# Kernel tuning notes

Hardware: AMD Instinct MI355X
Metric: run time of the kernel (lower is better)

## Reference

```python
import jax, jax.numpy as jnp
import numpy as np

L = 2048      # sequence length (self.len)
DIM = 1024    # model dim
DPOS = 128    # positional encoding dim
B = 4
EPS = 1e-5


def make_pe(length, d):
    # standard sinusoidal positional encoding, shape [length, d]
    pos = np.arange(length)[:, None].astype(np.float32)
    div = np.exp(-np.arange(0, d, 2).astype(np.float32) * (np.log(10000.0) / d))
    pe = np.zeros((length, d), dtype=np.float32)
    pe[:, 0::2] = np.sin(pos * div)
    pe[:, 1::2] = np.cos(pos * div)
    return jnp.asarray(pe)


def setup_inputs() -> dict:
    key = jax.random.key(0)
    ks = jax.random.split(key, 16)
    s = lambda fan_in: 1.0 / np.sqrt(fan_in)
    inp = {
        "z": jax.random.normal(ks[0], (B, L, DIM), jnp.float32),
        "x": jax.random.normal(ks[1], (B, L, DIM), jnp.float32),
        "a": jax.random.normal(ks[2], (1,), jnp.float32),
        "pe": make_pe(L, DPOS),
        # torch Linear weights stored [out, in]
        "w_pos1": jax.random.normal(ks[3], (DPOS + DIM, DPOS), jnp.float32) * s(DPOS),
        "b_pos1": jnp.zeros((DPOS + DIM,), jnp.float32),
        "w_pos2": jax.random.normal(ks[4], (DIM, DPOS + DIM), jnp.float32) * s(DPOS + DIM),
        "b_pos2": jnp.zeros((DIM,), jnp.float32),
        "w1": jax.random.normal(ks[5], (DIM * 2, DIM), jnp.float32) * s(DIM),
        "b1": jnp.zeros((DIM * 2,), jnp.float32),
        "w2": jax.random.normal(ks[6], (DIM, DIM * 2), jnp.float32) * s(DIM * 2),
        "b2": jnp.zeros((DIM,), jnp.float32),
        "w3": jax.random.normal(ks[7], (DIM * 2, DIM), jnp.float32) * s(DIM),
        "b3": jnp.zeros((DIM * 2,), jnp.float32),
        "w4": jax.random.normal(ks[8], (DIM, DIM * 2), jnp.float32) * s(DIM * 2),
        "b4": jnp.zeros((DIM,), jnp.float32),
        "ln_g": jnp.ones((DIM,), jnp.float32),
        "ln_b": jnp.zeros((DIM,), jnp.float32),
    }
    return inp


def _layer_norm(v, g, b):
    mu = jnp.mean(v, axis=-1, keepdims=True)
    var = jnp.var(v, axis=-1, keepdims=True)
    return (v - mu) * jax.lax.rsqrt(var + EPS) * g + b


def _lin(v, w, b):
    return v @ w.T + b


def reference(z, x, a, pe, w_pos1, b_pos1, w_pos2, b_pos2,
              w1, b1, w2, b2, w3, b3, w4, b4, ln_g, ln_b):
    zn = _layer_norm(z, ln_g, ln_b)                       # [B, L, D]
    fz = jnp.fft.rfft(zn, n=2 * L, axis=1)                # [B, L+1, D] complex
    expa = jnp.exp(a)                                     # [1]
    window = jnp.exp(-jnp.arange(L, dtype=jnp.float32) * expa)  # [L]
    h = _lin(pe, w_pos1, b_pos1)                          # [L, DPOS+D]
    h = jax.nn.gelu(h, approximate=False)
    h = _lin(h, w_pos2, b_pos2)                           # [L, D] (dropout eval = id)
    wfh = jnp.fft.rfft(window[:, None] * h, n=2 * L, axis=0)  # [L+1, D]
    cwhz = jnp.fft.irfft(wfh * fz, axis=1)[:, :L, :]      # [B, L, D]
    x1 = _lin(x, w1, b1)
    x1 = jax.nn.gelu(x1, approximate=False)
    x1 = _lin(x1, w2, b2)
    x1 = x1 * cwhz + z
    y = _layer_norm(x1, ln_g, ln_b)
    y = _lin(y, w3, b3)
    y = jax.nn.gelu(y, approximate=False)
    y = _lin(y, w4, b4)
    return y + x1
```

## Files before the change

### kernel.cpp

```cpp
#include <hip/hip_runtime.h>
#include <hip/hip_bf16.h>
#include <cmath>

typedef __hip_bfloat16 bf16;
typedef __attribute__((ext_vector_type(8))) short bf16x8;
typedef __attribute__((ext_vector_type(4))) float f32x4;

static __device__ __forceinline__ float b2f(bf16 v) { return __bfloat162float(v); }
static __device__ __forceinline__ bf16 f2b(float v) { return __float2bfloat16(v); }
static __device__ __forceinline__ float us2f(unsigned short u) {
  return __uint_as_float(((unsigned)u) << 16);
}

static __device__ __forceinline__ void gl2lds16(const bf16* g, bf16* l) {
  __builtin_amdgcn_global_load_lds(
      (const __attribute__((address_space(1))) void*)g,
      (__attribute__((address_space(3))) void*)l, 16, 0, 0);
}

static __device__ __forceinline__ float gelu_fast(float v) {
  float u = v * (0.7978845608f + 0.0356774081f * v * v);
  float e = __expf(2.f * u);
  return v * (e * __frcp_rn(e + 1.f));
}

static __device__ __forceinline__ int xcd_swz(int lid, int nwg) {
  const int q = nwg >> 3, r = nwg & 7;
  const int xcd = lid & 7, loc = lid >> 3;
  const int base = (xcd < r) ? xcd * (q + 1) : r * (q + 1) + (xcd - r) * q;
  return base + loc;
}

struct CvtSegs { const float* src[7]; int blk_off[8]; };
__global__ __launch_bounds__(256) void cvt7_k(CvtSegs s, bf16* __restrict__ dst0)
{
  int b = blockIdx.x;
  int seg = 0;
#pragma unroll
  for (int i = 0; i < 6; ++i) seg += (b >= s.blk_off[i + 1]) ? 1 : 0;
  const float* src = s.src[seg] + (size_t)(b - s.blk_off[seg]) * 1024;
  bf16* dst = dst0 + (size_t)b * 1024;
  int idx = threadIdx.x * 4;
  float4 v = *(const float4*)(src + idx);
  union { bf16 bb[4]; ushort4 u; } o;
  o.bb[0] = f2b(v.x); o.bb[1] = f2b(v.y); o.bb[2] = f2b(v.z); o.bb[3] = f2b(v.w);
  *(ushort4*)(dst + idx) = o.u;
}

__global__ __launch_bounds__(256) void cvt_k(const float* __restrict__ in,
                                             bf16* __restrict__ out, int n)
{
  int idx = (blockIdx.x * 256 + threadIdx.x) * 4;
  if (idx >= n) return;
  float4 v = *(const float4*)(in + idx);
  union { bf16 b[4]; ushort4 u; } o;
  o.b[0] = f2b(v.x); o.b[1] = f2b(v.y); o.b[2] = f2b(v.z); o.b[3] = f2b(v.w);
  *(ushort4*)(out + idx) = o.u;
}

__global__ __launch_bounds__(256) void ln_k(const float* __restrict__ X, bf16* __restrict__ Y,
                                            const float* __restrict__ gamma,
                                            const float* __restrict__ beta)
{
  __shared__ float red[16];
  const int row = blockIdx.x, tid = threadIdx.x;
  float4 v = *(const float4*)(X + (size_t)row * 1024 + tid * 4);
  float s  = v.x + v.y + v.z + v.w;
  float s2 = v.x * v.x + v.y * v.y + v.z * v.z + v.w * v.w;
#pragma unroll
  for (int m = 32; m; m >>= 1) { s += __shfl_xor(s, m, 64); s2 += __shfl_xor(s2, m, 64); }
  const int wid = tid >> 6;
  if ((tid & 63) == 0) { red[wid] = s; red[wid + 8] = s2; }
  __syncthreads();
  s  = red[0] + red[1] + red[2] + red[3];
  s2 = red[8] + red[9] + red[10] + red[11];
  const float mu  = s * (1.f / 1024.f);
  const float var = s2 * (1.f / 1024.f) - mu * mu;
  const float rs  = rsqrtf(var + 1e-5f);
  float4 g = *(const float4*)(gamma + tid * 4);
  float4 bt = *(const float4*)(beta + tid * 4);
  union { bf16 b[4]; ushort4 u; } o;
  o.b[0] = f2b((v.x - mu) * rs * g.x + bt.x);
  o.b[1] = f2b((v.y - mu) * rs * g.y + bt.y);
  o.b[2] = f2b((v.z - mu) * rs * g.z + bt.z);
  o.b[3] = f2b((v.w - mu) * rs * g.w + bt.w);
  *(ushort4*)(Y + (size_t)row * 1024 + tid * 4) = o.u;
}

template<int EPI>
__global__ __launch_bounds__(256, 3) void gemm_k(
    const bf16* __restrict__ A, const bf16* __restrict__ W,
    const float* __restrict__ bias, void* __restrict__ Out,
    const void* __restrict__ aux0, const void* __restrict__ aux1,
    int M, int N, int K)
{
  __shared__ bf16 As[3][128 * 32];
  __shared__ bf16 Bs[3][128 * 32];
  const int tid = threadIdx.x;
  const int wid = tid >> 6, lane = tid & 63;
  const int quad = lane >> 4, l16 = lane & 15;
  const int wm = wid >> 1, wn = wid & 1;

  const int nwg = gridDim.x * gridDim.y;
  int lid = xcd_swz(blockIdx.y * gridDim.x + blockIdx.x, nwg);
  const int bx = lid % gridDim.x, by = lid / gridDim.x;
  const int m0 = by * 128, n0 = bx * 128;

  f32x4 acc[4][4];
#pragma unroll
  for (int i = 0; i < 4; ++i)
#pragma unroll
    for (int j = 0; j < 4; ++j) acc[i][j] = (f32x4){0.f, 0.f, 0.f, 0.f};

  const bf16 *ga[2], *gb[2];
  int ldso[2];
#pragma unroll
  for (int r = 0; r < 2; ++r) {
    int p = r * 256 + wid * 64 + lane;
    int row = p >> 2;
    int sko = ((p & 3) ^ ((p >> 3) & 3)) << 3;
    ga[r] = A + (size_t)(m0 + row) * K + sko;
    gb[r] = W + (size_t)(n0 + row) * K + sko;
    ldso[r] = (r * 256 + wid * 64) * 8;
  }
  int apos[4], bpos[4];
#pragma unroll
  for (int i = 0; i < 4; ++i) {
    int ar = wm * 64 + i * 16 + l16;
    apos[i] = (ar * 4 + (quad ^ ((ar >> 1) & 3))) * 8;
    int br = wn * 64 + i * 16 + l16;
    bpos[i] = (br * 4 + (quad ^ ((br >> 1) & 3))) * 8;
  }

  const int niter = K >> 5;
#pragma unroll
  for (int t = 0; t < 2; ++t)
#pragma unroll
    for (int r = 0; r < 2; ++r) {
      gl2lds16(ga[r] + t * 32, &As[t][ldso[r]]);
      gl2lds16(gb[r] + t * 32, &Bs[t][ldso[r]]);
    }

  int cur = 0;
  for (int k = 0; k < niter; ++k) {
    if (k == niter - 1) { asm volatile("s_waitcnt vmcnt(0)" ::: "memory"); }
    else               { asm volatile("s_waitcnt vmcnt(4)" ::: "memory"); }
    asm volatile("s_barrier" ::: "memory");

    const bf16* as = As[cur];
    const bf16* bs = Bs[cur];
    bf16x8 af[4], bfr[4];
#pragma unroll
    for (int i = 0; i < 4; ++i) af[i]  = *(const bf16x8*)(as + apos[i]);
#pragma unroll
    for (int j = 0; j < 4; ++j) bfr[j] = *(const bf16x8*)(bs + bpos[j]);
    asm volatile("s_waitcnt lgkmcnt(0)" ::: "memory");

    if (k + 2 < niter) {
      int nb = cur + 2; if (nb >= 3) nb -= 3;
#pragma unroll
      for (int r = 0; r < 2; ++r) {
        gl2lds16(ga[r] + (k + 2) * 32, &As[nb][ldso[r]]);
        gl2lds16(gb[r] + (k + 2) * 32, &Bs[nb][ldso[r]]);
      }
    }
#pragma unroll
    for (int i = 0; i < 4; ++i)
#pragma unroll
      for (int j = 0; j < 4; ++j)
        acc[i][j] = __builtin_amdgcn_mfma_f32_16x16x32_bf16(af[i], bfr[j], acc[i][j], 0, 0, 0);
    cur += 1; if (cur == 3) cur = 0;
  }

  float expa = 0.f;
  if (EPI == 1) expa = expf(((const float*)aux0)[0]);
#pragma unroll
  for (int i = 0; i < 4; ++i) {
    const int gm_base = m0 + wm * 64 + i * 16 + quad * 4;
#pragma unroll
    for (int j = 0; j < 4; ++j) {
      const int gn = n0 + wn * 64 + j * 16 + l16;
      const float bv = bias[gn];
#pragma unroll
      for (int r = 0; r < 4; ++r) {
        const int gm = gm_base + r;
        const size_t off = (size_t)gm * N + gn;
        float v = acc[i][j][r] + bv;
        if (EPI == 0) ((bf16*)Out)[off] = f2b(gelu_fast(v));
        else if (EPI == 1) ((float*)Out)[off] = v * expf(-(float)gm * expa);
        else if (EPI == 2) ((float*)Out)[off] = v * ((const float*)aux0)[off] + ((const float*)aux1)[off];
        else ((float*)Out)[off] = v + ((const float*)aux0)[off];
      }
    }
  }
}

template<int EPI>
__global__ __launch_bounds__(256, 4) void gemm64_k(
    const bf16* __restrict__ A, const bf16* __restrict__ W,
    const float* __restrict__ bias, void* __restrict__ Out,
    const void* __restrict__ aux0, const void* __restrict__ aux1,
    int M, int N, int K)
{
  __shared__ bf16 As[3][128 * 32];
  __shared__ bf16 Bs[3][64 * 32];
  const int tid = threadIdx.x;
  const int wid = tid >> 6, lane = tid & 63;
  const int quad = lane >> 4, l16 = lane & 15;
  const int wm = wid >> 1, wn = wid & 1;

  const int nwg = gridDim.x * gridDim.y;
  int lid = xcd_swz(blockIdx.y * gridDim.x + blockIdx.x, nwg);
  const int bx = lid % gridDim.x, by = lid / gridDim.x;
  const int m0 = by * 128, n0 = bx * 64;

  f32x4 acc[4][2];
#pragma unroll
  for (int i = 0; i < 4; ++i)
#pragma unroll
    for (int j = 0; j < 2; ++j) acc[i][j] = (f32x4){0.f, 0.f, 0.f, 0.f};

  const bf16 *ga[2], *gbp;
  int ldsoA[2];
#pragma unroll
  for (int r = 0; r < 2; ++r) {
    int p = r * 256 + wid * 64 + lane;
    int row = p >> 2;
    int sko = ((p & 3) ^ ((p >> 3) & 3)) << 3;
    ga[r] = A + (size_t)(m0 + row) * K + sko;
    ldsoA[r] = (r * 256 + wid * 64) * 8;
  }
  {
    int p = wid * 64 + lane;
    int row = p >> 2;
    int sko = ((p & 3) ^ ((p >> 3) & 3)) << 3;
    gbp = W + (size_t)(n0 + row) * K + sko;
  }
  const int ldsoB = wid * 64 * 8;

  int apos[4], bpos[2];
#pragma unroll
  for (int i = 0; i < 4; ++i) {
    int ar = wm * 64 + i * 16 + l16;
    apos[i] = (ar * 4 + (quad ^ ((ar >> 1) & 3))) * 8;
  }
#pragma unroll
  for (int j = 0; j < 2; ++j) {
    int br = wn * 32 + j * 16 + l16;
    bpos[j] = (br * 4 + (quad ^ ((br >> 1) & 3))) * 8;
  }

  const int niter = K >> 5;
#pragma unroll
  for (int t = 0; t < 2; ++t) {
#pragma unroll
    for (int r = 0; r < 2; ++r) gl2lds16(ga[r] + t * 32, &As[t][ldsoA[r]]);
    gl2lds16(gbp + t * 32, &Bs[t][ldsoB]);
  }

  int cur = 0;
  for (int k = 0; k < niter; ++k) {
    if (k == niter - 1) { asm volatile("s_waitcnt vmcnt(0)" ::: "memory"); }
    else               { asm volatile("s_waitcnt vmcnt(3)" ::: "memory"); }
    asm volatile("s_barrier" ::: "memory");

    const bf16* as = As[cur];
    const bf16* bs = Bs[cur];
    bf16x8 af[4], bfr[2];
#pragma unroll
    for (int i = 0; i < 4; ++i) af[i]  = *(const bf16x8*)(as + apos[i]);
#pragma unroll
    for (int j = 0; j < 2; ++j) bfr[j] = *(const bf16x8*)(bs + bpos[j]);
    asm volatile("s_waitcnt lgkmcnt(0)" ::: "memory");

    if (k + 2 < niter) {
      int nb = cur + 2; if (nb >= 3) nb -= 3;
#pragma unroll
      for (int r = 0; r < 2; ++r) gl2lds16(ga[r] + (k + 2) * 32, &As[nb][ldsoA[r]]);
      gl2lds16(gbp + (k + 2) * 32, &Bs[nb][ldsoB]);
    }
#pragma unroll
    for (int i = 0; i < 4; ++i)
#pragma unroll
      for (int j = 0; j < 2; ++j)
        acc[i][j] = __builtin_amdgcn_mfma_f32_16x16x32_bf16(af[i], bfr[j], acc[i][j], 0, 0, 0);
    cur += 1; if (cur == 3) cur = 0;
  }

  float expa = 0.f;
  if (EPI == 1) expa = expf(((const float*)aux0)[0]);
#pragma unroll
  for (int i = 0; i < 4; ++i) {
    const int gm_base = m0 + wm * 64 + i * 16 + quad * 4;
#pragma unroll
    for (int j = 0; j < 2; ++j) {
      const int gn = n0 + wn * 32 + j * 16 + l16;
      const float bv = bias[gn];
#pragma unroll
      for (int r = 0; r < 4; ++r) {
        const int gm = gm_base + r;
        const size_t off = (size_t)gm * N + gn;
        float v = acc[i][j][r] + bv;
        if (EPI == 0) ((bf16*)Out)[off] = f2b(gelu_fast(v));
        else if (EPI == 1) ((float*)Out)[off] = v * expf(-(float)gm * expa);
        else if (EPI == 2) ((float*)Out)[off] = v * ((const float*)aux0)[off] + ((const float*)aux1)[off];
        else ((float*)Out)[off] = v + ((const float*)aux0)[off];
      }
    }
  }
}

__global__ __launch_bounds__(256) void conv_k(
    const bf16* __restrict__ zn,
    const float* __restrict__ wh,
    const float* __restrict__ a,
    float* __restrict__ out)
{
  __shared__ float whs[64 * 64];
  __shared__ float znt[128 * 64];
  const int tid = threadIdx.x;
  const int dd = tid & 63, ttg = tid >> 6;
  const int t0 = blockIdx.x * 64, d0 = blockIdx.y * 64, b = blockIdx.z;
  const float expa = expf(a[0]);
  const float smax = 20.7f / expa;
  const unsigned short* znu = (const unsigned short*)zn;

  float acc[16];
#pragma unroll
  for (int q = 0; q < 16; ++q) acc[q] = 0.f;

  for (int sb = 0; sb <= t0 + 63; sb += 64) {
    if ((float)sb > smax) break;
    float4 wv4[4];
#pragma unroll
    for (int i = 0; i < 4; ++i) {
      int cc = tid + 256 * i;
      int row = cc >> 4, dq = (cc & 15) * 4;
      wv4[i] = *(const float4*)&wh[(size_t)(sb + row) * 1024 + d0 + dq];
    }
    ushort4 zv4[8];
#pragma unroll
    for (int i = 0; i < 8; ++i) {
      int cc = tid + 256 * i;
      int row = cc >> 4, dq = (cc & 15) * 4;
      int u = t0 - sb - 64 + row;
      zv4[i] = (u >= 0) ? *(const ushort4*)&znu[((size_t)b * 2048 + u) * 1024 + d0 + dq]
                        : make_ushort4(0, 0, 0, 0);
    }
#pragma unroll
    for (int i = 0; i < 4; ++i) {
      int cc = tid + 256 * i;
      *(float4*)&whs[(cc >> 4) * 64 + (cc & 15) * 4] = wv4[i];
    }
#pragma unroll
    for (int i = 0; i < 8; ++i) {
      int cc = tid + 256 * i;
      float4 o;
      o.x = us2f(zv4[i].x); o.y = us2f(zv4[i].y); o.z = us2f(zv4[i].z); o.w = us2f(zv4[i].w);
      *(float4*)&znt[(cc >> 4) * 64 + (cc & 15) * 4] = o;
    }
    __syncthreads();

    float win[16];
#pragma unroll
    for (int q = 0; q < 16; ++q) win[q] = znt[(ttg * 16 + q + 64) * 64 + dd];
#pragma unroll
    for (int ss = 0; ss < 64; ++ss) {
      float wv = whs[ss * 64 + dd];
#pragma unroll
      for (int q = 0; q < 16; ++q) acc[q] += wv * win[q];
      if (ss < 63) {
#pragma unroll
        for (int q = 15; q >= 1; --q) win[q] = win[q - 1];
        win[0] = znt[(ttg * 16 + 63 - ss) * 64 + dd];
      }
    }
    __syncthreads();
  }
#pragma unroll
  for (int q = 0; q < 16; ++q) {
    int t = t0 + ttg * 16 + q;
    out[((size_t)b * 2048 + t) * 1024 + d0 + dd] = acc[q];
  }
}

extern "C" void kernel_launch(void* const* d_in, const int* in_sizes, int n_in,
                              void* d_out, int out_size, void* d_ws, size_t ws_size,
                              hipStream_t stream)
{
  const float* z      = (const float*)d_in[0];
  const float* x      = (const float*)d_in[1];
  const float* a      = (const float*)d_in[2];
  const float* pe     = (const float*)d_in[3];
  const float* w_pos1 = (const float*)d_in[4];
  const float* b_pos1 = (const float*)d_in[5];
  const float* w_pos2 = (const float*)d_in[6];
  const float* b_pos2 = (const float*)d_in[7];
  const float* w1     = (const float*)d_in[8];
  const float* b1     = (const float*)d_in[9];
  const float* w2     = (const float*)d_in[10];
  const float* b2     = (const float*)d_in[11];
  const float* w3     = (const float*)d_in[12];
  const float* b3     = (const float*)d_in[13];
  const float* w4     = (const float*)d_in[14];
  const float* b4     = (const float*)d_in[15];
  const float* ln_g   = (const float*)d_in[16];
  const float* ln_b   = (const float*)d_in[17];

  char* ws = (char*)d_ws;
  bf16* pe_bf  = (bf16*)(ws + 0);
  bf16* wp1_bf = (bf16*)(ws + 524288);
  bf16* wp2_bf = (bf16*)(ws + 819200);
  bf16* w1_bf  = (bf16*)(ws + 3178496);
  bf16* w2_bf  = (bf16*)(ws + 7372800);
  bf16* w3_bf  = (bf16*)(ws + 11567104);
  bf16* w4_bf  = (bf16*)(ws + 15761408);
  bf16* h1     = (bf16*)(ws + 19955712);
  bf16* zn_bf  = (bf16*)(ws + 24674304);
  bf16* x_bf   = (bf16*)(ws + 41451520);
  float* wh    = (float*)(ws + 58228736);
  float* cwhz  = (float*)(ws + 66617344);
  bf16*  x1n   = (bf16*)(ws + 66617344);
  bf16*  g     = (bf16*)(ws + 100171776);
  float* x1    = (float*)(ws + 24674304);
  float* out   = (float*)d_out;

  CvtSegs segs;
  segs.src[0] = pe;  segs.src[1] = w_pos1; segs.src[2] = w_pos2;
  segs.src[3] = w1;  segs.src[4] = w2;     segs.src[5] = w3; segs.src[6] = w4;
  int bo[8] = {0, 256, 400, 1552, 3600, 5648, 7696, 9744};
  for (int i = 0; i < 8; ++i) segs.blk_off[i] = bo[i];
  cvt7_k<<<9744, 256, 0, stream>>>(segs, (bf16*)ws);
  cvt_k<<<8192, 256, 0, stream>>>(x, x_bf, 8388608);

  ln_k<<<8192, 256, 0, stream>>>(z, zn_bf, ln_g, ln_b);
  gemm_k<0><<<dim3(9, 16), 256, 0, stream>>>(pe_bf, wp1_bf, b_pos1, h1, nullptr, nullptr, 2048, 1152, 128);
  gemm64_k<1><<<dim3(16, 16), 256, 0, stream>>>(h1, wp2_bf, b_pos2, wh, a, nullptr, 2048, 1024, 1152);
  conv_k<<<dim3(32, 16, 4), 256, 0, stream>>>(zn_bf, wh, a, cwhz);
  gemm_k<0><<<dim3(16, 64), 256, 0, stream>>>(x_bf, w1_bf, b1, g, nullptr, nullptr, 8192, 2048, 1024);
  gemm64_k<2><<<dim3(16, 64), 256, 0, stream>>>(g, w2_bf, b2, x1, cwhz, z, 8192, 1024, 2048);
  ln_k<<<8192, 256, 0, stream>>>(x1, x1n, ln_g, ln_b);
  gemm_k<0><<<dim3(16, 64), 256, 0, stream>>>(x1n, w3_bf, b3, g, nullptr, nullptr, 8192, 2048, 1024);
  gemm64_k<3><<<dim3(16, 64), 256, 0, stream>>>(g, w4_bf, b4, out, x1, nullptr, 8192, 1024, 2048);
}
```

Before: 444.3 us.

## Replace narrow 128x64 GEMM with 128x128 BK=64 double-buffered kernel for big GEMMs

```diff
diff --git a/kernel.cpp b/kernel.cpp
--- a/kernel.cpp
+++ b/kernel.cpp
@@ -196,14 +196,14 @@
 }
 
 template<int EPI>
-__global__ __launch_bounds__(256, 4) void gemm64_k(
+__global__ __launch_bounds__(256, 2) void gemmw_k(
     const bf16* __restrict__ A, const bf16* __restrict__ W,
     const float* __restrict__ bias, void* __restrict__ Out,
     const void* __restrict__ aux0, const void* __restrict__ aux1,
     int M, int N, int K)
 {
-  __shared__ bf16 As[3][128 * 32];
-  __shared__ bf16 Bs[3][64 * 32];
+  __shared__ bf16 As[2][128 * 64];
+  __shared__ bf16 Bs[2][128 * 64];
   const int tid = threadIdx.x;
   const int wid = tid >> 6, lane = tid & 63;
   const int quad = lane >> 4, l16 = lane & 15;
@@ -212,79 +212,77 @@
   const int nwg = gridDim.x * gridDim.y;
   int lid = xcd_swz(blockIdx.y * gridDim.x + blockIdx.x, nwg);
   const int bx = lid % gridDim.x, by = lid / gridDim.x;
-  const int m0 = by * 128, n0 = bx * 64;
-
-  f32x4 acc[4][2];
+  const int m0 = by * 128, n0 = bx * 128;
+
+  f32x4 acc[4][4];
 #pragma unroll
   for (int i = 0; i < 4; ++i)
 #pragma unroll
-    for (int j = 0; j < 2; ++j) acc[i][j] = (f32x4){0.f, 0.f, 0.f, 0.f};
-
-  const bf16 *ga[2], *gbp;
-  int ldsoA[2];
-#pragma unroll
-  for (int r = 0; r < 2; ++r) {
-    int p = r * 256 + wid * 64 + lane;
-    int row = p >> 2;
-    int sko = ((p & 3) ^ ((p >> 3) & 3)) << 3;
-    ga[r] = A + (size_t)(m0 + row) * K + sko;
-    ldsoA[r] = (r * 256 + wid * 64) * 8;
-  }
-  {
-    int p = wid * 64 + lane;
-    int row = p >> 2;
-    int sko = ((p & 3) ^ ((p >> 3) & 3)) << 3;
-    gbp = W + (size_t)(n0 + row) * K + sko;
-  }
-  const int ldsoB = wid * 64 * 8;
-
-  int apos[4], bpos[2];
+    for (int j = 0; j < 4; ++j) acc[i][j] = (f32x4){0.f, 0.f, 0.f, 0.f};
+
+  const bf16 *ga[4], *gb[4];
+  int ldso[4];
+#pragma unroll
+  for (int r = 0; r < 4; ++r) {
+    int p = r * 256 + tid;
+    int row = p >> 3;
+    int c = (p & 7) ^ (row & 7);
+    ga[r] = A + (size_t)(m0 + row) * K + c * 8;
+    gb[r] = W + (size_t)(n0 + row) * K + c * 8;
+    ldso[r] = p * 8;
+  }
+  int apos[4][2], bpos[4][2];
 #pragma unroll
   for (int i = 0; i < 4; ++i) {
     int ar = wm * 64 + i * 16 + l16;
-    apos[i] = (ar * 4 + (quad ^ ((ar >> 1) & 3))) * 8;
-  }
-#pragma unroll
-  for (int j = 0; j < 2; ++j) {
-    int br = wn * 32 + j * 16 + l16;
-    bpos[j] = (br * 4 + (quad ^ ((br >> 1) & 3))) * 8;
-  }
-
-  const int niter = K >> 5;
-#pragma unroll
-  for (int t = 0; t < 2; ++t) {
-#pragma unroll
-    for (int r = 0; r < 2; ++r) gl2lds16(ga[r] + t * 32, &As[t][ldsoA[r]]);
-    gl2lds16(gbp + t * 32, &Bs[t][ldsoB]);
-  }
-
-  int cur = 0;
+    int br = wn * 64 + i * 16 + l16;
+#pragma unroll
+    for (int ks = 0; ks < 2; ++ks) {
+      apos[i][ks] = ar * 64 + (((quad + 4 * ks) ^ (ar & 7)) * 8);
+      bpos[i][ks] = br * 64 + (((quad + 4 * ks) ^ (br & 7)) * 8);
+    }
+  }
+
+  const int niter = K >> 6;
+
+#pragma unroll
+  for (int r = 0; r < 4; ++r) {
+    gl2lds16(ga[r], &As[0][ldso[r]]);
+    gl2lds16(gb[r], &Bs[0][ldso[r]]);
+  }
+
   for (int k = 0; k < niter; ++k) {
-    if (k == niter - 1) { asm volatile("s_waitcnt vmcnt(0)" ::: "memory"); }
-    else               { asm volatile("s_waitcnt vmcnt(3)" ::: "memory"); }
+    asm volatile("s_waitcnt vmcnt(0)" ::: "memory");
     asm volatile("s_barrier" ::: "memory");
-
+    const int cur = k & 1;
+    if (k + 1 < niter) {
+      const int nxt = cur ^ 1;
+#pragma unroll
+      for (int r = 0; r < 4; ++r) {
+        gl2lds16(ga[r] + (k + 1) * 64, &As[nxt][ldso[r]]);
+        gl2lds16(gb[r] + (k + 1) * 64, &Bs[nxt][ldso[r]]);
+      }
+    }
     const bf16* as = As[cur];
     const bf16* bs = Bs[cur];
-    bf16x8 af[4], bfr[2];
-#pragma unroll
-    for (int i = 0; i < 4; ++i) af[i]  = *(const bf16x8*)(as + apos[i]);
-#pragma unroll
-    for (int j = 0; j < 2; ++j) bfr[j] = *(const bf16x8*)(bs + bpos[j]);
+    bf16x8 af[4][2], bfr[4][2];
+#pragma unroll
+    for (int i = 0; i < 4; ++i)
+#pragma unroll
+      for (int ks = 0; ks < 2; ++ks) af[i][ks] = *(const bf16x8*)(as + apos[i][ks]);
+#pragma unroll
+    for (int j = 0; j < 4; ++j)
+#pragma unroll
+      for (int ks = 0; ks < 2; ++ks) bfr[j][ks] = *(const bf16x8*)(bs + bpos[j][ks]);
     asm volatile("s_waitcnt lgkmcnt(0)" ::: "memory");
 
-    if (k + 2 < niter) {
-      int nb = cur + 2; if (nb >= 3) nb -= 3;
-#pragma unroll
-      for (int r = 0; r < 2; ++r) gl2lds16(ga[r] + (k + 2) * 32, &As[nb][ldsoA[r]]);
-      gl2lds16(gbp + (k + 2) * 32, &Bs[nb][ldsoB]);
-    }
-#pragma unroll
-    for (int i = 0; i < 4; ++i)
-#pragma unroll
-      for (int j = 0; j < 2; ++j)
-        acc[i][j] = __builtin_amdgcn_mfma_f32_16x16x32_bf16(af[i], bfr[j], acc[i][j], 0, 0, 0);
-    cur += 1; if (cur == 3) cur = 0;
+#pragma unroll
+    for (int ks = 0; ks < 2; ++ks)
+#pragma unroll
+      for (int i = 0; i < 4; ++i)
+#pragma unroll
+        for (int j = 0; j < 4; ++j)
+          acc[i][j] = __builtin_amdgcn_mfma_f32_16x16x32_bf16(af[i][ks], bfr[j][ks], acc[i][j], 0, 0, 0);
   }
 
   float expa = 0.f;
@@ -293,8 +291,8 @@
   for (int i = 0; i < 4; ++i) {
     const int gm_base = m0 + wm * 64 + i * 16 + quad * 4;
 #pragma unroll
-    for (int j = 0; j < 2; ++j) {
-      const int gn = n0 + wn * 32 + j * 16 + l16;
+    for (int j = 0; j < 4; ++j) {
+      const int gn = n0 + wn * 64 + j * 16 + l16;
       const float bv = bias[gn];
 #pragma unroll
       for (int r = 0; r < 4; ++r) {
@@ -435,11 +433,11 @@
 
   ln_k<<<8192, 256, 0, stream>>>(z, zn_bf, ln_g, ln_b);
   gemm_k<0><<<dim3(9, 16), 256, 0, stream>>>(pe_bf, wp1_bf, b_pos1, h1, nullptr, nullptr, 2048, 1152, 128);
-  gemm64_k<1><<<dim3(16, 16), 256, 0, stream>>>(h1, wp2_bf, b_pos2, wh, a, nullptr, 2048, 1024, 1152);
+  gemmw_k<1><<<dim3(8, 16), 256, 0, stream>>>(h1, wp2_bf, b_pos2, wh, a, nullptr, 2048, 1024, 1152);
   conv_k<<<dim3(32, 16, 4), 256, 0, stream>>>(zn_bf, wh, a, cwhz);
-  gemm_k<0><<<dim3(16, 64), 256, 0, stream>>>(x_bf, w1_bf, b1, g, nullptr, nullptr, 8192, 2048, 1024);
-  gemm64_k<2><<<dim3(16, 64), 256, 0, stream>>>(g, w2_bf, b2, x1, cwhz, z, 8192, 1024, 2048);
+  gemmw_k<0><<<dim3(16, 64), 256, 0, stream>>>(x_bf, w1_bf, b1, g, nullptr, nullptr, 8192, 2048, 1024);
+  gemmw_k<2><<<dim3(8, 64), 256, 0, stream>>>(g, w2_bf, b2, x1, cwhz, z, 8192, 1024, 2048);
   ln_k<<<8192, 256, 0, stream>>>(x1, x1n, ln_g, ln_b);
-  gemm_k<0><<<dim3(16, 64), 256, 0, stream>>>(x1n, w3_bf, b3, g, nullptr, nullptr, 8192, 2048, 1024);
-  gemm64_k<3><<<dim3(16, 64), 256, 0, stream>>>(g, w4_bf, b4, out, x1, nullptr, 8192, 1024, 2048);
-}
+  gemmw_k<0><<<dim3(16, 64), 256, 0, stream>>>(x1n, w3_bf, b3, g, nullptr, nullptr, 8192, 2048, 1024);
+  gemmw_k<3><<<dim3(8, 64), 256, 0, stream>>>(g, w4_bf, b4, out, x1, nullptr, 8192, 1024, 2048);
+}
```

Result: faster. 424.5 us (-4.4%).
